# Optimization experiments

Hardware: AMD Instinct MI355X
Metric: run time of the kernel (lower is better)

## Reference

```python
import jax, jax.numpy as jnp
import numpy as np

NP_, B_ = 44, 400000

def setup_inputs() -> dict:
    key = jax.random.key(0)
    k_x, k1, k2, k3, k4 = jax.random.split(key, 5)
    return {
        "X": jax.random.normal(k_x, (NP_, 1, B_), dtype=jnp.float32),
        "lin1s": jax.random.normal(k1, (NP_, 4, 1), dtype=jnp.float32),
        "lin2s": jax.random.normal(k2, (NP_, 8, 4), dtype=jnp.float32),
        "lin3s": jax.random.normal(k3, (NP_, 4, 8), dtype=jnp.float32),
        "lin4s": jax.random.normal(k4, (NP_, 1, 4), dtype=jnp.float32),
    }

def reference(X, lin1s, lin2s, lin3s, lin4s):
    # forward_all: chained batched tiny GEMMs with ReLU, 'lik,lkj->lij'
    h = jax.nn.relu(jnp.einsum('lik,lkj->lij', lin1s, X))   # (NP, 4, B)
    h = jax.nn.relu(jnp.einsum('lik,lkj->lij', lin2s, h))   # (NP, 8, B)
    h = jax.nn.relu(jnp.einsum('lik,lkj->lij', lin3s, h))   # (NP, 4, B)
    return jnp.einsum('lik,lkj->lij', lin4s, h)             # (NP, 1, B)
```

## Files before the change

kernel.cpp:

```cpp
#include <hip/hip_runtime.h>

#define NP  44
#define B   400000
#define B4  (B / 4)
#define BLK 256
#define CPT 8

typedef float v4f __attribute__((ext_vector_type(4)));

__device__ __forceinline__ void collapse_weights(
    const float* __restrict__ p1, const float* __restrict__ p2,
    const float* __restrict__ p3, const float* __restrict__ p4,
    float& gp, float& gn)
{
    float w1p[4], w1n[4];
#pragma unroll
    for (int k = 0; k < 4; ++k) {
        float w = p1[k];
        w1p[k] = fmaxf(w, 0.0f);
        w1n[k] = fminf(w, 0.0f);
    }

    float d2p[8], d2n[8];
#pragma unroll
    for (int i = 0; i < 8; ++i) {
        float ap = 0.0f, an = 0.0f;
#pragma unroll
        for (int k = 0; k < 4; ++k) {
            float w = p2[i * 4 + k];
            ap = fmaf(w, w1p[k], ap);
            an = fmaf(w, w1n[k], an);
        }
        d2p[i] = fmaxf(ap, 0.0f);
        d2n[i] = fminf(an, 0.0f);
    }

    float f3p[4], f3n[4];
#pragma unroll
    for (int j = 0; j < 4; ++j) {
        float ap = 0.0f, an = 0.0f;
#pragma unroll
        for (int i = 0; i < 8; ++i) {
            float w = p3[j * 8 + i];
            ap = fmaf(w, d2p[i], ap);
            an = fmaf(w, d2n[i], an);
        }
        f3p[j] = fmaxf(ap, 0.0f);
        f3n[j] = fminf(an, 0.0f);
    }

    gp = 0.0f; gn = 0.0f;
#pragma unroll
    for (int j = 0; j < 4; ++j) {
        gp = fmaf(p4[j], f3p[j], gp);
        gn = fmaf(p4[j], f3n[j], gn);
    }
}

__device__ __forceinline__ v4f scale4(v4f v, float gp, float gn) {
    v4f r;
    r.x = v.x * (v.x >= 0.0f ? gp : gn);
    r.y = v.y * (v.y >= 0.0f ? gp : gn);
    r.z = v.z * (v.z >= 0.0f ? gp : gn);
    r.w = v.w * (v.w >= 0.0f ? gp : gn);
    return r;
}

__global__ __launch_bounds__(BLK) void collapsed_mlp_kernel(
    const float* __restrict__ X,
    const float* __restrict__ W1,
    const float* __restrict__ W2,
    const float* __restrict__ W3,
    const float* __restrict__ W4,
    float* __restrict__ out)
{
    const int l    = blockIdx.y;
    const int base = blockIdx.x * (BLK * CPT) + threadIdx.x;

    const v4f* Xp = (const v4f*)(X + (size_t)l * B);
    v4f*       Op = (v4f*)(out + (size_t)l * B);

    const bool full = (blockIdx.x + 1) * (BLK * CPT) <= B4;

    v4f xv[CPT];
    if (full) {
#pragma unroll
        for (int c = 0; c < CPT; ++c) xv[c] = Xp[base + c * BLK];
    }

    float gp, gn;
    collapse_weights(W1 + l * 4, W2 + l * 32, W3 + l * 32, W4 + l * 4, gp, gn);

    if (full) {
#pragma unroll
        for (int c = 0; c < CPT; ++c) {
            __builtin_nontemporal_store(scale4(xv[c], gp, gn), &Op[base + c * BLK]);
        }
    } else {
#pragma unroll
        for (int c = 0; c < CPT; ++c) {
            const int idx = base + c * BLK;
            if (idx < B4) {
                v4f v = Xp[idx];
                __builtin_nontemporal_store(scale4(v, gp, gn), &Op[idx]);
            }
        }
    }
}

extern "C" void kernel_launch(void* const* d_in, const int* in_sizes, int n_in,
                              void* d_out, int out_size, void* d_ws, size_t ws_size,
                              hipStream_t stream) {
    const float* X  = (const float*)d_in[0];
    const float* W1 = (const float*)d_in[1];
    const float* W2 = (const float*)d_in[2];
    const float* W3 = (const float*)d_in[3];
    const float* W4 = (const float*)d_in[4];
    float* out = (float*)d_out;

    dim3 grid((B4 + BLK * CPT - 1) / (BLK * CPT), NP);
    collapsed_mlp_kernel<<<grid, BLK, 0, stream>>>(X, W1, W2, W3, W4, out);
}
```

Baseline: 127.6 us.

## Precompute collapsed weights in a separate kernel and grid-stride the streaming pass

After: 128.2 us. Within noise of the previous version (+0.5%).

```diff
diff --git a/kernel.cpp b/kernel.cpp
--- a/kernel.cpp
+++ b/kernel.cpp
@@ -1,18 +1,27 @@
 #include <hip/hip_runtime.h>
 
-#define NP  44
-#define B   400000
-#define B4  (B / 4)
-#define BLK 256
-#define CPT 8
+#define NP    44
+#define B     400000
+#define B4    (B / 4)
+#define BLK   256
+#define GX    46
+#define STRIDE (GX * BLK)
+#define FULL_ITERS 8
 
 typedef float v4f __attribute__((ext_vector_type(4)));
 
-__device__ __forceinline__ void collapse_weights(
-    const float* __restrict__ p1, const float* __restrict__ p2,
-    const float* __restrict__ p3, const float* __restrict__ p4,
-    float& gp, float& gn)
+__global__ __launch_bounds__(64) void collapse_kernel(
+    const float* __restrict__ W1, const float* __restrict__ W2,
+    const float* __restrict__ W3, const float* __restrict__ W4,
+    float2* __restrict__ g)
 {
+    const int l = threadIdx.x;
+    if (l >= NP) return;
+    const float* p1 = W1 + l * 4;
+    const float* p2 = W2 + l * 32;
+    const float* p3 = W3 + l * 32;
+    const float* p4 = W4 + l * 4;
+
     float w1p[4], w1n[4];
 #pragma unroll
     for (int k = 0; k < 4; ++k) {
@@ -20,7 +29,6 @@
         w1p[k] = fmaxf(w, 0.0f);
         w1n[k] = fminf(w, 0.0f);
     }
-
     float d2p[8], d2n[8];
 #pragma unroll
     for (int i = 0; i < 8; ++i) {
@@ -34,7 +42,6 @@
         d2p[i] = fmaxf(ap, 0.0f);
         d2n[i] = fminf(an, 0.0f);
     }
-
     float f3p[4], f3n[4];
 #pragma unroll
     for (int j = 0; j < 4; ++j) {
@@ -48,13 +55,13 @@
         f3p[j] = fmaxf(ap, 0.0f);
         f3n[j] = fminf(an, 0.0f);
     }
-
-    gp = 0.0f; gn = 0.0f;
+    float gp = 0.0f, gn = 0.0f;
 #pragma unroll
     for (int j = 0; j < 4; ++j) {
         gp = fmaf(p4[j], f3p[j], gp);
         gn = fmaf(p4[j], f3n[j], gn);
     }
+    g[l] = make_float2(gp, gn);
 }
 
 __device__ __forceinline__ v4f scale4(v4f v, float gp, float gn) {
@@ -66,44 +73,31 @@
     return r;
 }
 
-__global__ __launch_bounds__(BLK) void collapsed_mlp_kernel(
+__global__ __launch_bounds__(BLK) void stream_kernel(
     const float* __restrict__ X,
-    const float* __restrict__ W1,
-    const float* __restrict__ W2,
-    const float* __restrict__ W3,
-    const float* __restrict__ W4,
+    const float2* __restrict__ g,
     float* __restrict__ out)
 {
-    const int l    = blockIdx.y;
-    const int base = blockIdx.x * (BLK * CPT) + threadIdx.x;
+    const int l = blockIdx.y;
+    const float2 gg = g[l];
+    const float gp = gg.x, gn = gg.y;
 
     const v4f* Xp = (const v4f*)(X + (size_t)l * B);
     v4f*       Op = (v4f*)(out + (size_t)l * B);
 
-    const bool full = (blockIdx.x + 1) * (BLK * CPT) <= B4;
+    const int base = blockIdx.x * BLK + threadIdx.x;
 
-    v4f xv[CPT];
-    if (full) {
 #pragma unroll
-        for (int c = 0; c < CPT; ++c) xv[c] = Xp[base + c * BLK];
+    for (int it = 0; it < FULL_ITERS; ++it) {
+        const int idx = base + it * STRIDE;
+        v4f v = Xp[idx];
+        Op[idx] = scale4(v, gp, gn);
     }
-
-    float gp, gn;
-    collapse_weights(W1 + l * 4, W2 + l * 32, W3 + l * 32, W4 + l * 4, gp, gn);
-
-    if (full) {
-#pragma unroll
-        for (int c = 0; c < CPT; ++c) {
-            __builtin_nontemporal_store(scale4(xv[c], gp, gn), &Op[base + c * BLK]);
-        }
-    } else {
-#pragma unroll
-        for (int c = 0; c < CPT; ++c) {
-            const int idx = base + c * BLK;
-            if (idx < B4) {
-                v4f v = Xp[idx];
-                __builtin_nontemporal_store(scale4(v, gp, gn), &Op[idx]);
-            }
+    {
+        const int idx = base + FULL_ITERS * STRIDE;
+        if (idx < B4) {
+            v4f v = Xp[idx];
+            Op[idx] = scale4(v, gp, gn);
         }
     }
 }
@@ -117,7 +111,8 @@
     const float* W3 = (const float*)d_in[3];
     const float* W4 = (const float*)d_in[4];
     float* out = (float*)d_out;
+    float2* g = (float2*)d_ws;
 
-    dim3 grid((B4 + BLK * CPT - 1) / (BLK * CPT), NP);
-    collapsed_mlp_kernel<<<grid, BLK, 0, stream>>>(X, W1, W2, W3, W4, out);
+    collapse_kernel<<<dim3(1), 64, 0, stream>>>(W1, W2, W3, W4, g);
+    stream_kernel<<<dim3(GX, NP), BLK, 0, stream>>>(X, g, out);
 }
```
